# Performance work log

Hardware: AMD Instinct MI355X
Metric: run time of the kernel (lower is better)

Reference implementation:

```python
import jax, jax.numpy as jnp
import numpy as np

B, S, D, H = 2, 2048, 1024, 16
HD = D // H
SCALE = HD ** -0.5
NEG = -1e30


def setup_inputs() -> dict:
    key = jax.random.key(0)
    ks = jax.random.split(key, 10)
    w = lambda k: jax.random.normal(k, (D, D), dtype=jnp.float32) * 0.02
    b = lambda k: jax.random.normal(k, (D,), dtype=jnp.float32) * 0.01
    hidden_states = jax.random.normal(ks[0], (B, S, D), dtype=jnp.float32)
    document_ids = jnp.sort(jax.random.randint(ks[1], (S,), 0, 16))
    return {
        'hidden_states': hidden_states,
        'wq': w(ks[2]), 'bq': b(ks[3]),
        'wk': w(ks[4]), 'bk': b(ks[5]),
        'wv': w(ks[6]), 'bv': b(ks[7]),
        'wo': w(ks[8]), 'bo': b(ks[9]),
        'document_ids': document_ids,
    }


def reference(hidden_states, wq, bq, wk, bk, wv, bv, wo, bo, document_ids):
    # projections (nn.Linear: x @ W.T + b)
    q = (hidden_states @ wq.T + bq).reshape(B, S, H, HD)
    k = (hidden_states @ wk.T + bk).reshape(B, S, H, HD)
    v = (hidden_states @ wv.T + bv).reshape(B, S, H, HD)
    # document-block mask: attend only within same document
    mask = document_ids[:, None] == document_ids[None, :]  # [S, S]
    scores = jnp.einsum('bqhd,bkhd->bhqk', q, k) * SCALE
    scores = jnp.where(mask[None, None], scores, NEG)
    attn = jax.nn.softmax(scores, axis=-1)
    out = jnp.einsum('bhqk,bkhd->bqhd', attn, v).reshape(B, S, D)
    return out @ wo.T + bo
```

## Files before the change

kernel.cpp:

```cpp
#include <hip/hip_runtime.h>
#include <hip/hip_bf16.h>
#include <math.h>

#define B 2
#define S 2048
#define D 1024
#define H 16
#define HD 64
#define SCALE 0.125f
#define NEGBIG -1e30f

#define NE 4194304
#define NW 1048576
#define NE8 524288
#define NW8 131072

typedef _Float16 f16;
typedef _Float16 f16x8 __attribute__((ext_vector_type(8)));
typedef _Float16 f16x4 __attribute__((ext_vector_type(4)));
typedef float f32x4  __attribute__((ext_vector_type(4)));

__device__ __forceinline__ void gl_lds16(const void* g, void* l) {
    __builtin_amdgcn_global_load_lds(
        (const __attribute__((address_space(1))) unsigned int*)g,
        (__attribute__((address_space(3))) unsigned int*)l, 16, 0, 0);
}

__device__ __forceinline__ void wave_lds_fence() {
    __builtin_amdgcn_wave_barrier();
    __builtin_amdgcn_s_waitcnt(0xC07F);
    __builtin_amdgcn_wave_barrier();
}

__global__ __launch_bounds__(256) void prep_k(
    const float4* __restrict__ hs,
    const float4* __restrict__ wq, const float4* __restrict__ wk,
    const float4* __restrict__ wv, const float4* __restrict__ wo,
    const int* __restrict__ doc,
    f16x8* __restrict__ xh, f16x8* __restrict__ wqkv, f16x8* __restrict__ woh,
    int* __restrict__ dstart, int* __restrict__ dend)
{
    int i = blockIdx.x * blockDim.x + threadIdx.x;
    if (i < NE8 + 4 * NW8) {
        const float4* src;
        f16x8* dst;
        if (i < NE8) { src = hs + 2 * (size_t)i; dst = xh + i; }
        else {
            int j = i - NE8;
            int id = j / NW8, jj = j - id * NW8;
            src = ((id == 0) ? wq : (id == 1) ? wk : (id == 2) ? wv : wo) + 2 * (size_t)jj;
            dst = (id < 3) ? (wqkv + (size_t)id * NW8 + jj) : (woh + jj);
        }
        float4 a = src[0], b = src[1];
        f16x8 h;
        h[0] = (f16)a.x; h[1] = (f16)a.y; h[2] = (f16)a.z; h[3] = (f16)a.w;
        h[4] = (f16)b.x; h[5] = (f16)b.y; h[6] = (f16)b.z; h[7] = (f16)b.w;
        *dst = h;
    } else {
        int s = i - (NE8 + 4 * NW8);
        if (s < S) {
            int v = doc[s];
            int lo = 0, hi = S;
            while (lo < hi) { int mid = (lo + hi) >> 1; if (doc[mid] < v) lo = mid + 1; else hi = mid; }
            dstart[s] = lo;
            lo = 0; hi = S;
            while (lo < hi) { int mid = (lo + hi) >> 1; if (doc[mid] <= v) lo = mid + 1; else hi = mid; }
            dend[s] = lo;
        }
    }
}

__global__ __launch_bounds__(256) void qkv_mfma_k(
    const f16* __restrict__ xh, const f16* __restrict__ wqkv,
    const float* __restrict__ bq, const float* __restrict__ bk,
    const float* __restrict__ bv,
    f16* __restrict__ Qh, f16* __restrict__ Kh, f16* __restrict__ Vth)
{
    __shared__ union {
        struct { f16 Ah[128 * 64]; f16 Bh[128 * 64]; } s;
        f16 tr[64 * 136];
    } lds;

    const int which = blockIdx.z;
    const f16* Bhg = wqkv + (size_t)which * D * D;

    const int tid = threadIdx.x;
    const int w = tid >> 6, ln = tid & 63;
    const int wm = (w & 1) * 64, wn = (w >> 1) * 64;
    const int lc = ln & 15, quad = ln >> 4;
    const int m0 = blockIdx.y * 128, n0 = blockIdx.x * 128;

    f32x4 acc[4][4];
    #pragma unroll
    for (int i = 0; i < 4; i++)
        #pragma unroll
        for (int j = 0; j < 4; j++) acc[i][j] = (f32x4){0.f, 0.f, 0.f, 0.f};

    for (int k0 = 0; k0 < 1024; k0 += 64) {
        #pragma unroll
        for (int i = 0; i < 4; i++) {
            int rl = w * 32 + i * 8 + (ln >> 3);
            int oc = (ln & 7) ^ (rl & 7);
            size_t ga = (size_t)(m0 + rl) * 1024 + k0 + oc * 8;
            size_t gb = (size_t)(n0 + rl) * 1024 + k0 + oc * 8;
            int lofs = (w * 32 + i * 8) * 64;
            gl_lds16(xh + ga, lds.s.Ah + lofs);
            gl_lds16(Bhg + gb, lds.s.Bh + lofs);
        }
        __syncthreads();

        #pragma unroll
        for (int ks = 0; ks < 2; ks++) {
            f16x8 ah[4], bh[4];
            #pragma unroll
            for (int t = 0; t < 4; t++) {
                int am = wm + t * 16 + lc;
                ah[t] = *(const f16x8*)&lds.s.Ah[am * 64 + (((ks * 4 + quad) ^ (am & 7)) * 8)];
                int bn = wn + t * 16 + lc;
                bh[t] = *(const f16x8*)&lds.s.Bh[bn * 64 + (((ks * 4 + quad) ^ (bn & 7)) * 8)];
            }
            #pragma unroll
            for (int mt = 0; mt < 4; mt++)
                #pragma unroll
                for (int nt = 0; nt < 4; nt++)
                    acc[mt][nt] = __builtin_amdgcn_mfma_f32_16x16x32_f16(ah[mt], bh[nt], acc[mt][nt], 0, 0, 0);
        }
        __syncthreads();
    }

    if (which < 2) {
        const float* bias = (which == 0) ? bq : bk;
        #pragma unroll
        for (int nt = 0; nt < 4; nt++) {
            int col = n0 + wn + nt * 16 + lc;
            float bv_ = bias[col];
            int h = col >> 6, hd = col & 63;
            #pragma unroll
            for (int mt = 0; mt < 4; mt++) {
                #pragma unroll
                for (int r = 0; r < 4; r++) {
                    int m = m0 + wm + mt * 16 + quad * 4 + r;
                    int bbm = m >> 11, s = m & (S - 1);
                    float val = acc[mt][nt][r] + bv_;
                    if (which == 0) val *= SCALE;
                    size_t idx = (((size_t)(bbm * H + h) * S) + s) * HD + hd;
                    ((which == 0) ? Qh : Kh)[idx] = (f16)val;
                }
            }
        }
    } else {
        const int bb = m0 >> 11;
        const int sbase = m0 & (S - 1);
        #pragma unroll
        for (int pass = 0; pass < 2; pass++) {
            if ((w >> 1) == pass) {
                #pragma unroll
                for (int nt = 0; nt < 4; nt++) {
                    int colp = nt * 16 + lc;
                    float bv_ = bv[n0 + pass * 64 + colp];
                    #pragma unroll
                    for (int mt = 0; mt < 4; mt++) {
                        f16x4 v;
                        #pragma unroll
                        for (int r = 0; r < 4; r++) v[r] = (f16)(acc[mt][nt][r] + bv_);
                        *(f16x4*)&lds.tr[colp * 136 + wm + mt * 16 + quad * 4] = v;
                    }
                }
            }
            __syncthreads();
            #pragma unroll
            for (int p2 = 0; p2 < 4; p2++) {
                int chunk = tid + p2 * 256;
                int colp = chunk >> 4;
                int oct = chunk & 15;
                f16x8 v = *(const f16x8*)&lds.tr[colp * 136 + oct * 8];
                int vcol = n0 + pass * 64 + colp;
                int h = vcol >> 6, hd = vcol & 63;
                size_t idx = (((size_t)(bb * H + h) * HD) + hd) * S + sbase + oct * 8;
                *(f16x8*)(Vth + idx) = v;
            }
            __syncthreads();
        }
    }
}

__global__ __launch_bounds__(256) void out_mfma_k(
    const f16* __restrict__ oh, const f16* __restrict__ wh,
    const float* __restrict__ bias, float* __restrict__ Y)
{
    __shared__ f16 Ah[128 * 64], Bh[64 * 64];
    const int tid = threadIdx.x;
    const int w = tid >> 6, ln = tid & 63;
    const int wm = (w & 1) * 64, wn = (w >> 1) * 32;
    const int lc = ln & 15, quad = ln >> 4;
    const int m0 = blockIdx.y * 128, n0 = blockIdx.x * 64;

    f32x4 acc[4][2];
    #pragma unroll
    for (int i = 0; i < 4; i++)
        #pragma unroll
        for (int j = 0; j < 2; j++) acc[i][j] = (f32x4){0.f, 0.f, 0.f, 0.f};

    for (int k0 = 0; k0 < 1024; k0 += 64) {
        #pragma unroll
        for (int i = 0; i < 4; i++) {
            int rl = w * 32 + i * 8 + (ln >> 3);
            int oc = (ln & 7) ^ (rl & 7);
            gl_lds16(oh + (size_t)(m0 + rl) * 1024 + k0 + oc * 8, Ah + (w * 32 + i * 8) * 64);
        }
        #pragma unroll
        for (int i = 0; i < 2; i++) {
            int rl = w * 16 + i * 8 + (ln >> 3);
            int oc = (ln & 7) ^ (rl & 7);
            gl_lds16(wh + (size_t)(n0 + rl) * 1024 + k0 + oc * 8, Bh + (w * 16 + i * 8) * 64);
        }
        __syncthreads();

        #pragma unroll
        for (int ks = 0; ks < 2; ks++) {
            f16x8 ah[4], bh[2];
            #pragma unroll
            for (int t = 0; t < 4; t++) {
                int am = wm + t * 16 + lc;
                ah[t] = *(const f16x8*)&Ah[am * 64 + (((ks * 4 + quad) ^ (am & 7)) * 8)];
            }
            #pragma unroll
            for (int t = 0; t < 2; t++) {
                int bn = wn + t * 16 + lc;
                bh[t] = *(const f16x8*)&Bh[bn * 64 + (((ks * 4 + quad) ^ (bn & 7)) * 8)];
            }
            #pragma unroll
            for (int mt = 0; mt < 4; mt++)
                #pragma unroll
                for (int nt = 0; nt < 2; nt++)
                    acc[mt][nt] = __builtin_amdgcn_mfma_f32_16x16x32_f16(ah[mt], bh[nt], acc[mt][nt], 0, 0, 0);
        }
        __syncthreads();
    }

    #pragma unroll
    for (int nt = 0; nt < 2; nt++) {
        int col = n0 + wn + nt * 16 + lc;
        float bv_ = bias[col];
        #pragma unroll
        for (int mt = 0; mt < 4; mt++) {
            #pragma unroll
            for (int r = 0; r < 4; r++) {
                int m = m0 + wm + mt * 16 + quad * 4 + r;
                Y[(size_t)m * D + col] = acc[mt][nt][r] + bv_;
            }
        }
    }
}

__device__ __forceinline__ void load_kfrag(
    const f16* __restrict__ Kh, size_t bh, int j0, int lc, int quad, f16x8 kf[4][2])
{
    #pragma unroll
    for (int t = 0; t < 4; t++) {
        size_t krow = (bh + j0 + t * 16 + lc) * HD;
        #pragma unroll
        for (int ks = 0; ks < 2; ks++)
            kf[t][ks] = *(const f16x8*)(Kh + krow + ks * 32 + quad * 8);
    }
}

__global__ __launch_bounds__(256) void attn4_k(
    const f16* __restrict__ Qh, const f16* __restrict__ Kh,
    const f16* __restrict__ Vth,
    const int* __restrict__ dstart, const int* __restrict__ dend,
    f16* __restrict__ Ohi)
{
    const int qt = blockIdx.x, h = blockIdx.y, b = blockIdx.z;
    const int tid = threadIdx.x;
    const int w = tid >> 6, ln = tid & 63;
    const int lc = ln & 15, quad = ln >> 4;
    const int q0 = qt * 64 + w * 16;
    const size_t bh  = ((size_t)b * H + h) * S;
    const size_t bhv = ((size_t)b * H + h) * HD;

    __shared__ float Ps[4][2][16 * 65];

    int row_st[4], row_en[4];
    #pragma unroll
    for (int r = 0; r < 4; r++) {
        row_st[r] = dstart[q0 + quad * 4 + r];
        row_en[r] = dend[q0 + quad * 4 + r];
    }
    const int kstart = dstart[q0] & ~63;
    const int kend   = dend[q0 + 15];

    const size_t qrow = bh + q0 + lc;
    f16x8 qf[2];
    #pragma unroll
    for (int ks = 0; ks < 2; ks++)
        qf[ks] = *(const f16x8*)(Qh + qrow * HD + ks * 32 + quad * 8);

    f32x4 o[4];
    #pragma unroll
    for (int nt = 0; nt < 4; nt++) o[nt] = (f32x4){0.f, 0.f, 0.f, 0.f};
    f32x4 m_i = (f32x4){NEGBIG, NEGBIG, NEGBIG, NEGBIG};
    f32x4 l_i = (f32x4){0.f, 0.f, 0.f, 0.f};

    f16x8 kf[4][2], kf2[4][2];
    load_kfrag(Kh, bh, kstart, lc, quad, kf);

    int it = 0;
    for (int j0 = kstart; j0 < kend; j0 += 64, it ^= 1) {
        float* ps = &Ps[w][it][0];
        const bool more = (j0 + 64) < kend;
        if (more) load_kfrag(Kh, bh, j0 + 64, lc, quad, kf2);

        f32x4 sc[4];
        #pragma unroll
        for (int t = 0; t < 4; t++) {
            f32x4 a = (f32x4){0.f, 0.f, 0.f, 0.f};
            #pragma unroll
            for (int ks = 0; ks < 2; ks++)
                a = __builtin_amdgcn_mfma_f32_16x16x32_f16(qf[ks], kf[t][ks], a, 0, 0, 0);
            int key = j0 + t * 16 + lc;
            #pragma unroll
            for (int r = 0; r < 4; r++) {
                bool valid = (key >= row_st[r]) && (key < row_en[r]);
                sc[t][r] = valid ? a[r] : NEGBIG;
            }
        }

        f32x4 mx = sc[0];
        #pragma unroll
        for (int t = 1; t < 4; t++)
            #pragma unroll
            for (int r = 0; r < 4; r++) mx[r] = fmaxf(mx[r], sc[t][r]);
        #pragma unroll
        for (int off = 1; off <= 8; off <<= 1)
            #pragma unroll
            for (int r = 0; r < 4; r++) mx[r] = fmaxf(mx[r], __shfl_xor(mx[r], off, 64));

        f32x4 m_new, alpha;
        #pragma unroll
        for (int r = 0; r < 4; r++) {
            m_new[r] = fmaxf(m_i[r], mx[r]);
            alpha[r] = __expf(m_i[r] - m_new[r]);
        }

        f32x4 psum = (f32x4){0.f, 0.f, 0.f, 0.f};
        f32x4 pv[4];
        #pragma unroll
        for (int t = 0; t < 4; t++) {
            #pragma unroll
            for (int r = 0; r < 4; r++) {
                float p = __expf(sc[t][r] - m_new[r]);
                p = (sc[t][r] < -5e29f) ? 0.f : p;
                pv[t][r] = p;
                psum[r] += p;
            }
        }
        #pragma unroll
        for (int off = 1; off <= 8; off <<= 1)
            #pragma unroll
            for (int r = 0; r < 4; r++) psum[r] += __shfl_xor(psum[r], off, 64);

        #pragma unroll
        for (int r = 0; r < 4; r++) {
            l_i[r] = l_i[r] * alpha[r] + psum[r];
            m_i[r] = m_new[r];
        }
        #pragma unroll
        for (int nt = 0; nt < 4; nt++)
            #pragma unroll
            for (int r = 0; r < 4; r++) o[nt][r] *= alpha[r];

        f16x8 vh[2][4];
        #pragma unroll
        for (int ks = 0; ks < 2; ks++) {
            int gp = ks * 4 + quad;
            #pragma unroll
            for (int nt = 0; nt < 4; nt++) {
                int dim = nt * 16 + lc;
                vh[ks][nt] = *(const f16x8*)(Vth + (bhv + dim) * S + j0 + gp * 8);
            }
        }

        #pragma unroll
        for (int t = 0; t < 4; t++) {
            int g = 2 * t + (lc >> 3);
            #pragma unroll
            for (int r = 0; r < 4; r++) {
                int q = quad * 4 + r;
                ps[q * 65 + ((g ^ (q & 7)) * 8) + (lc & 7)] = pv[t][r];
            }
        }

        wave_lds_fence();

        #pragma unroll
        for (int ks = 0; ks < 2; ks++) {
            int gp = ks * 4 + quad;
            const float* prow = &ps[lc * 65 + ((gp ^ (lc & 7)) * 8)];
            f16x8 ph;
            #pragma unroll
            for (int j = 0; j < 8; j++) ph[j] = (f16)prow[j];
            #pragma unroll
            for (int nt = 0; nt < 4; nt++)
                o[nt] = __builtin_amdgcn_mfma_f32_16x16x32_f16(ph, vh[ks][nt], o[nt], 0, 0, 0);
        }

        if (more) {
            #pragma unroll
            for (int t = 0; t < 4; t++)
                #pragma unroll
                for (int ks = 0; ks < 2; ks++) kf[t][ks] = kf2[t][ks];
        }
    }

    f32x4 inv;
    #pragma unroll
    for (int r = 0; r < 4; r++) inv[r] = 1.f / l_i[r];
    #pragma unroll
    for (int nt = 0; nt < 4; nt++) {
        int dim = nt * 16 + lc;
        #pragma unroll
        for (int r = 0; r < 4; r++) {
            int q = q0 + quad * 4 + r;
            float val = o[nt][r] * inv[r];
            size_t idx = ((size_t)(b * S + q)) * D + h * 64 + dim;
            Ohi[idx] = (f16)val;
        }
    }
}

extern "C" void kernel_launch(void* const* d_in, const int* in_sizes, int n_in,
                              void* d_out, int out_size, void* d_ws, size_t ws_size,
                              hipStream_t stream) {
    const float* hs = (const float*)d_in[0];
    const float* wq = (const float*)d_in[1];
    const float* bq = (const float*)d_in[2];
    const float* wk = (const float*)d_in[3];
    const float* bk = (const float*)d_in[4];
    const float* wv = (const float*)d_in[5];
    const float* bv = (const float*)d_in[6];
    const float* wo = (const float*)d_in[7];
    const float* bo = (const float*)d_in[8];
    const int*  doc = (const int*)d_in[9];
    float* out = (float*)d_out;

    f16* xh   = (f16*)d_ws;
    f16* Qhb  = xh + NE;
    f16* Khb  = Qhb + NE;
    f16* Vth  = Khb + NE;
    f16* wqkv = Vth + NE;
    f16* woh  = wqkv + 3 * (size_t)NW;
    int* dstart = (int*)(woh + NW);
    int* dend = dstart + S;

    prep_k<<<(NE8 + 4 * NW8 + S + 255) / 256, 256, 0, stream>>>(
        (const float4*)hs, (const float4*)wq, (const float4*)wk,
        (const float4*)wv, (const float4*)wo, doc,
        (f16x8*)xh, (f16x8*)wqkv, (f16x8*)woh, dstart, dend);

    qkv_mfma_k<<<dim3(D / 128, (B * S) / 128, 3), 256, 0, stream>>>(
        xh, wqkv, bq, bk, bv, Qhb, Khb, Vth);
    attn4_k<<<dim3(S / 64, H, B), 256, 0, stream>>>(
        Qhb, Khb, Vth, dstart, dend, xh);
    out_mfma_k<<<dim3(D / 64, (B * S) / 128), 256, 0, stream>>>(xh, woh, bo, out);
}
```

Before: 194.6 us.

## Double-buffer QKV GEMM with 256x256 tiles and 512-thread blocks

```diff
diff --git a/kernel.cpp b/kernel.cpp
--- a/kernel.cpp
+++ b/kernel.cpp
@@ -70,110 +70,155 @@
     }
 }
 
-__global__ __launch_bounds__(256) void qkv_mfma_k(
+__global__ __launch_bounds__(512, 2) void qkv_mfma_k(
     const f16* __restrict__ xh, const f16* __restrict__ wqkv,
     const float* __restrict__ bq, const float* __restrict__ bk,
     const float* __restrict__ bv,
     f16* __restrict__ Qh, f16* __restrict__ Kh, f16* __restrict__ Vth)
 {
     __shared__ union {
-        struct { f16 Ah[128 * 64]; f16 Bh[128 * 64]; } s;
-        f16 tr[64 * 136];
+        struct { f16 At[2][256 * 64]; f16 Bt[2][256 * 64]; } s;
+        f16 tr[64 * 264];
     } lds;
 
     const int which = blockIdx.z;
-    const f16* Bhg = wqkv + (size_t)which * D * D;
+    const f16* Bg = wqkv + (size_t)which * D * D;
 
     const int tid = threadIdx.x;
     const int w = tid >> 6, ln = tid & 63;
-    const int wm = (w & 1) * 64, wn = (w >> 1) * 64;
+    const int wm = (w & 1) * 128, wn = (w >> 1) * 64;
     const int lc = ln & 15, quad = ln >> 4;
-    const int m0 = blockIdx.y * 128, n0 = blockIdx.x * 128;
-
-    f32x4 acc[4][4];
-    #pragma unroll
-    for (int i = 0; i < 4; i++)
+    const int m0 = blockIdx.y * 256, n0 = blockIdx.x * 256;
+
+    size_t aoff[4], boff[4];
+    int ldst[4];
+    #pragma unroll
+    for (int i = 0; i < 4; i++) {
+        int r = w * 32 + i * 8 + (ln >> 3);
+        int o = (ln & 7) ^ (r & 7);
+        aoff[i] = (size_t)(m0 + r) * 1024 + o * 8;
+        boff[i] = (size_t)(n0 + r) * 1024 + o * 8;
+        ldst[i] = (w * 32 + i * 8) * 64;
+    }
+
+    f32x4 acc[8][4];
+    #pragma unroll
+    for (int i = 0; i < 8; i++)
         #pragma unroll
         for (int j = 0; j < 4; j++) acc[i][j] = (f32x4){0.f, 0.f, 0.f, 0.f};
 
-    for (int k0 = 0; k0 < 1024; k0 += 64) {
-        #pragma unroll
-        for (int i = 0; i < 4; i++) {
-            int rl = w * 32 + i * 8 + (ln >> 3);
-            int oc = (ln & 7) ^ (rl & 7);
-            size_t ga = (size_t)(m0 + rl) * 1024 + k0 + oc * 8;
-            size_t gb = (size_t)(n0 + rl) * 1024 + k0 + oc * 8;
-            int lofs = (w * 32 + i * 8) * 64;
-            gl_lds16(xh + ga, lds.s.Ah + lofs);
-            gl_lds16(Bhg + gb, lds.s.Bh + lofs);
-        }
-        __syncthreads();
-
-        #pragma unroll
-        for (int ks = 0; ks < 2; ks++) {
-            f16x8 ah[4], bh[4];
+    #define STAGE(buf, k0) { \
+        f16* Ad_ = lds.s.At[buf]; f16* Bd_ = lds.s.Bt[buf]; \
+        _Pragma("unroll") \
+        for (int i_ = 0; i_ < 4; i_++) gl_lds16(xh + aoff[i_] + (k0), Ad_ + ldst[i_]); \
+        _Pragma("unroll") \
+        for (int i_ = 0; i_ < 4; i_++) gl_lds16(Bg + boff[i_] + (k0), Bd_ + ldst[i_]); }
+
+    STAGE(0, 0)
+    STAGE(1, 64)
+    asm volatile("s_waitcnt vmcnt(8)");
+    __builtin_amdgcn_sched_barrier(0);
+    __builtin_amdgcn_s_barrier();
+    __builtin_amdgcn_sched_barrier(0);
+
+    for (int kt = 0; kt < 16; ++kt) {
+        const int cur = kt & 1;
+        const f16* Acur = lds.s.At[cur];
+        const f16* Bcur = lds.s.Bt[cur];
+
+        #pragma unroll
+        for (int q = 0; q < 4; ++q) {
+            f16x8 af[2][2], bf[4][2];
+            #pragma unroll
+            for (int t = 0; t < 2; t++) {
+                int am = wm + (q * 2 + t) * 16 + lc;
+                #pragma unroll
+                for (int ks = 0; ks < 2; ks++)
+                    af[t][ks] = *(const f16x8*)&Acur[am * 64 + (((ks * 4 + quad) ^ (am & 7)) * 8)];
+            }
             #pragma unroll
             for (int t = 0; t < 4; t++) {
-                int am = wm + t * 16 + lc;
-                ah[t] = *(const f16x8*)&lds.s.Ah[am * 64 + (((ks * 4 + quad) ^ (am & 7)) * 8)];
                 int bn = wn + t * 16 + lc;
-                bh[t] = *(const f16x8*)&lds.s.Bh[bn * 64 + (((ks * 4 + quad) ^ (bn & 7)) * 8)];
-            }
-            #pragma unroll
-            for (int mt = 0; mt < 4; mt++)
-                #pragma unroll
-                for (int nt = 0; nt < 4; nt++)
-                    acc[mt][nt] = __builtin_amdgcn_mfma_f32_16x16x32_f16(ah[mt], bh[nt], acc[mt][nt], 0, 0, 0);
-        }
-        __syncthreads();
-    }
+                #pragma unroll
+                for (int ks = 0; ks < 2; ks++)
+                    bf[t][ks] = *(const f16x8*)&Bcur[bn * 64 + (((ks * 4 + quad) ^ (bn & 7)) * 8)];
+            }
+            __builtin_amdgcn_s_setprio(1);
+            #pragma unroll
+            for (int ks = 0; ks < 2; ks++)
+                #pragma unroll
+                for (int mt = 0; mt < 2; mt++)
+                    #pragma unroll
+                    for (int nt = 0; nt < 4; nt++)
+                        acc[q * 2 + mt][nt] = __builtin_amdgcn_mfma_f32_16x16x32_f16(
+                            af[mt][ks], bf[nt][ks], acc[q * 2 + mt][nt], 0, 0, 0);
+            __builtin_amdgcn_s_setprio(0);
+        }
+
+        if (kt == 15) break;
+
+        __builtin_amdgcn_s_barrier();
+        __builtin_amdgcn_sched_barrier(0);
+        if (kt + 2 < 16) {
+            STAGE(cur, (kt + 2) * 64)
+            asm volatile("s_waitcnt vmcnt(8)");
+        } else {
+            asm volatile("s_waitcnt vmcnt(0)");
+        }
+        __builtin_amdgcn_sched_barrier(0);
+        __builtin_amdgcn_s_barrier();
+        __builtin_amdgcn_sched_barrier(0);
+    }
+    #undef STAGE
 
     if (which < 2) {
         const float* bias = (which == 0) ? bq : bk;
+        f16* dst = (which == 0) ? Qh : Kh;
         #pragma unroll
         for (int nt = 0; nt < 4; nt++) {
             int col = n0 + wn + nt * 16 + lc;
-            float bv_ = bias[col];
+            float bias_v = bias[col];
             int h = col >> 6, hd = col & 63;
             #pragma unroll
-            for (int mt = 0; mt < 4; mt++) {
+            for (int mt = 0; mt < 8; mt++) {
                 #pragma unroll
                 for (int r = 0; r < 4; r++) {
                     int m = m0 + wm + mt * 16 + quad * 4 + r;
                     int bbm = m >> 11, s = m & (S - 1);
-                    float val = acc[mt][nt][r] + bv_;
+                    float val = acc[mt][nt][r] + bias_v;
                     if (which == 0) val *= SCALE;
                     size_t idx = (((size_t)(bbm * H + h) * S) + s) * HD + hd;
-                    ((which == 0) ? Qh : Kh)[idx] = (f16)val;
+                    dst[idx] = (f16)val;
                 }
             }
         }
     } else {
         const int bb = m0 >> 11;
         const int sbase = m0 & (S - 1);
-        #pragma unroll
-        for (int pass = 0; pass < 2; pass++) {
+        __syncthreads();
+        #pragma unroll
+        for (int pass = 0; pass < 4; pass++) {
             if ((w >> 1) == pass) {
                 #pragma unroll
                 for (int nt = 0; nt < 4; nt++) {
                     int colp = nt * 16 + lc;
-                    float bv_ = bv[n0 + pass * 64 + colp];
+                    float bvv = bv[n0 + pass * 64 + colp];
                     #pragma unroll
-                    for (int mt = 0; mt < 4; mt++) {
+                    for (int mt = 0; mt < 8; mt++) {
                         f16x4 v;
                         #pragma unroll
-                        for (int r = 0; r < 4; r++) v[r] = (f16)(acc[mt][nt][r] + bv_);
-                        *(f16x4*)&lds.tr[colp * 136 + wm + mt * 16 + quad * 4] = v;
+                        for (int r = 0; r < 4; r++) v[r] = (f16)(acc[mt][nt][r] + bvv);
+                        *(f16x4*)&lds.tr[colp * 264 + wm + mt * 16 + quad * 4] = v;
                     }
                 }
             }
             __syncthreads();
             #pragma unroll
             for (int p2 = 0; p2 < 4; p2++) {
-                int chunk = tid + p2 * 256;
-                int colp = chunk >> 4;
-                int oct = chunk & 15;
-                f16x8 v = *(const f16x8*)&lds.tr[colp * 136 + oct * 8];
+                int chunk = tid + p2 * 512;
+                int colp = chunk >> 5;
+                int oct = chunk & 31;
+                f16x8 v = *(const f16x8*)&lds.tr[colp * 264 + oct * 8];
                 int vcol = n0 + pass * 64 + colp;
                 int h = vcol >> 6, hd = vcol & 63;
                 size_t idx = (((size_t)(bb * H + h) * HD) + hd) * S + sbase + oct * 8;
@@ -458,7 +503,7 @@
         (const float4*)wv, (const float4*)wo, doc,
         (f16x8*)xh, (f16x8*)wqkv, (f16x8*)woh, dstart, dend);
 
-    qkv_mfma_k<<<dim3(D / 128, (B * S) / 128, 3), 256, 0, stream>>>(
+    qkv_mfma_k<<<dim3(D / 256, (B * S) / 256, 3), 512, 0, stream>>>(
         xh, wqkv, bq, bk, bv, Qhb, Khb, Vth);
     attn4_k<<<dim3(S / 64, H, B), 256, 0, stream>>>(
         Qhb, Khb, Vth, dstart, dend, xh);
```

After: 187.9 us. -3.4%, faster.
